# Performance work log

Measured on AMD Instinct MI355X. Metric: run time of the kernel, lower is better.

The kernel has to match this reference:

```python
import jax, jax.numpy as jnp
import numpy as np

C = 256

def _conv1x1(x, w, b):
    # x: [B,C,H,W], w: [O,I], b: [O]  (1x1 conv == pointwise GEMM over channels)
    return jnp.einsum('oi,bihw->bohw', w, x) + b[None, :, None, None]

def setup_inputs() -> dict:
    key = jax.random.key(0)
    ks = jax.random.split(key, 9)
    s = 1.0 / np.sqrt(C)
    x = jax.random.normal(ks[0], (16, C, 64, 64), dtype=jnp.float32)
    wf = jax.random.uniform(ks[1], (C, C), jnp.float32, -s, s)
    bf = jax.random.uniform(ks[2], (C,), jnp.float32, -s, s)
    wg = jax.random.uniform(ks[3], (C, C), jnp.float32, -s, s)
    bg = jax.random.uniform(ks[4], (C,), jnp.float32, -s, s)
    wh = jax.random.uniform(ks[5], (C, C), jnp.float32, -s, s)
    bh = jax.random.uniform(ks[6], (C,), jnp.float32, -s, s)
    wv = jax.random.uniform(ks[7], (C, C), jnp.float32, -s, s)
    bv = jax.random.uniform(ks[8], (C,), jnp.float32, -s, s)
    return {"x": x, "wf": wf, "bf": bf, "wg": wg, "bg": bg,
            "wh": wh, "bh": bh, "wv": wv, "bv": bv}

def reference(x, wf, bf, wg, bg, wh, bh, wv, bv):
    fx = _conv1x1(x, wf, bf)              # [B,C,H,W]
    gx = _conv1x1(x, wg, bg)              # [B,C,H,W]
    # scores: fx^T @ gx over spatial H -> [B,C,W,W]
    scores = jnp.einsum('bchw,bchv->bcwv', fx, gx)
    attn = jax.nn.softmax(scores, axis=-1)  # softmax over last W dim
    hx = _conv1x1(x, wh, bh)              # [B,C,H,W]
    out = jnp.einsum('bchw,bcwv->bchv', hx, attn)  # hx @ attn -> [B,C,H,W]
    return _conv1x1(out, wv, bv)
```

## Files before the change

### kernel.cpp

```cpp
#include <hip/hip_runtime.h>
#include <math.h>

#define CH  256
#define SPA 4096
#define BB  16
#define PLANE 16777216

typedef _Float16 f16x8 __attribute__((ext_vector_type(8)));
typedef _Float16 f16x4 __attribute__((ext_vector_type(4)));
typedef float    f32x4 __attribute__((ext_vector_type(4)));

__device__ __forceinline__ void gload16(const void* g, void* l) {
    __builtin_amdgcn_global_load_lds(
        (const __attribute__((address_space(1))) unsigned int*)g,
        (__attribute__((address_space(3))) unsigned int*)l, 16, 0, 0);
}

__global__ __launch_bounds__(256) void xpose_kernel(
    const float* __restrict__ src, _Float16* __restrict__ dst)
{
    __shared__ float T[64][65];
    const int t  = threadIdx.x;
    const int b  = blockIdx.x >> 8;
    const int st = (blockIdx.x >> 2) & 63;
    const int rt = blockIdx.x & 3;
    const int s0 = st << 6, r0 = rt << 6;

    #pragma unroll
    for (int p = 0; p < 4; ++p) {
        int k = (t >> 4) + (p << 4);
        float4 v = *(const float4*)(src + (((size_t)((b << 8) + r0 + k)) << 12)
                                        + s0 + ((t & 15) << 2));
        T[k][((t & 15) << 2) + 0] = v.x;
        T[k][((t & 15) << 2) + 1] = v.y;
        T[k][((t & 15) << 2) + 2] = v.z;
        T[k][((t & 15) << 2) + 3] = v.w;
    }
    __syncthreads();

    const int s  = t >> 2;
    const int kg = (t & 3) << 4;
    const size_t obase = (((size_t)((b << 12) + s0 + s)) << 8) + r0 + kg;

    f16x8 h0, h1;
    #pragma unroll
    for (int i = 0; i < 16; ++i) {
        _Float16 hv = (_Float16)T[kg + i][s];
        if (i < 8) h0[i] = hv; else h1[i - 8] = hv;
    }
    *(f16x8*)(dst + obase)     = h0;
    *(f16x8*)(dst + obase + 8) = h1;
}

__global__ __launch_bounds__(256) void cpose_kernel(
    const _Float16* __restrict__ src, _Float16* __restrict__ dst)
{
    __shared__ _Float16 T[64][68];
    const int t  = threadIdx.x;
    const int b  = blockIdx.x >> 8;
    const int st = (blockIdx.x >> 2) & 63;
    const int ct = blockIdx.x & 3;
    const int s0 = st << 6, c0 = ct << 6;

    #pragma unroll
    for (int p = 0; p < 4; ++p) {
        int fi = (p << 8) + t;
        int r = fi >> 4, s4 = (fi & 15) << 2;
        f16x4 v = *(const f16x4*)(src + (((size_t)((b << 8) + c0 + r)) << 12) + s0 + s4);
        *(f16x4*)&T[r][s4] = v;
    }
    __syncthreads();

    const int s  = t >> 2;
    const int cg = (t & 3) << 4;
    f16x8 h0, h1;
    #pragma unroll
    for (int i = 0; i < 16; ++i) {
        _Float16 hv = T[cg + i][s];
        if (i < 8) h0[i] = hv; else h1[i - 8] = hv;
    }
    const size_t obase = (((size_t)((b << 12) + s0 + s)) << 8) + c0 + cg;
    *(f16x8*)(dst + obase)     = h0;
    *(f16x8*)(dst + obase + 8) = h1;
}

__global__ __launch_bounds__(256) void wcvt_kernel(
    const float* __restrict__ w0, const float* __restrict__ w1,
    const float* __restrict__ w2, const float* __restrict__ w3,
    _Float16* __restrict__ dst)
{
    const int idx = blockIdx.x * 256 + threadIdx.x;
    dst[idx]             = (_Float16)w0[idx];
    dst[65536 + idx]     = (_Float16)w1[idx];
    dst[131072 + idx]    = (_Float16)w2[idx];
    dst[196608 + idx]    = (_Float16)w3[idx];
}

__global__ __launch_bounds__(256) void gemm_fgh_kernel(
    const _Float16* __restrict__ xT, const _Float16* __restrict__ wc,
    const float* __restrict__ bias0, const float* __restrict__ bias1,
    const float* __restrict__ bias2, _Float16* __restrict__ outp)
{
    __shared__ _Float16 S[10240];
    _Float16* sA = S;

    const int tid = threadIdx.x;
    const int w = tid >> 6, lane = tid & 63, q = lane >> 4, li = lane & 15;
    const int r_ = blockIdx.x;
    const int ot    = r_ & 3;
    const int stile = (r_ >> 2) & 31;
    const int b     = r_ >> 7;
    const int s0 = stile << 7, o0 = ot << 6;

    const float* biases[3] = {bias0, bias1, bias2};

    f32x4 acc[3][4][2];
    #pragma unroll
    for (int m = 0; m < 3; ++m)
        #pragma unroll
        for (int t2 = 0; t2 < 4; ++t2)
            #pragma unroll
            for (int u = 0; u < 2; ++u) acc[m][t2][u] = (f32x4){0.f, 0.f, 0.f, 0.f};

    const int rr = tid >> 2;
    const int cc = (tid & 3) << 3;

    const int n0 = (w & 1) << 5;
    const int m0 = (w >> 1) << 6;

    for (int kb = 0; kb < CH; kb += 32) {
        __syncthreads();
        {
            const size_t ga = (((size_t)((b << 12) + s0 + rr)) << 8) + kb + cc;
            gload16(xT + ga, sA + tid * 8);
            gload16(xT + ga + (64ull << 8), sA + 2048 + tid * 8);
            #pragma unroll
            for (int m = 0; m < 3; ++m) {
                const size_t gb = (((size_t)(o0 + rr)) << 8) + m * 65536 + kb + cc;
                gload16(wc + gb, S + 4096 + m * 2048 + tid * 8);
            }
        }
        __syncthreads();

        f16x8 a[4];
        #pragma unroll
        for (int t2 = 0; t2 < 4; ++t2)
            a[t2] = *(const f16x8*)(sA + (m0 + (t2 << 4) + li) * 32 + (q << 3));

        #pragma unroll
        for (int m = 0; m < 3; ++m) {
            const _Float16* sB = S + 4096 + m * 2048;
            f16x8 b0 = *(const f16x8*)(sB + (n0 + li) * 32 + (q << 3));
            f16x8 b1 = *(const f16x8*)(sB + (n0 + 16 + li) * 32 + (q << 3));
            #pragma unroll
            for (int t2 = 0; t2 < 4; ++t2) {
                acc[m][t2][0] = __builtin_amdgcn_mfma_f32_16x16x32_f16(a[t2], b0, acc[m][t2][0], 0, 0, 0);
                acc[m][t2][1] = __builtin_amdgcn_mfma_f32_16x16x32_f16(a[t2], b1, acc[m][t2][1], 0, 0, 0);
            }
        }
    }

    #pragma unroll
    for (int m = 0; m < 3; ++m) {
        _Float16* ob = outp + (size_t)m * PLANE;
        #pragma unroll
        for (int u = 0; u < 2; ++u) {
            const int o = o0 + n0 + (u << 4) + li;
            const float bz = biases[m][o];
            #pragma unroll
            for (int t2 = 0; t2 < 4; ++t2) {
                const int s = s0 + m0 + (t2 << 4) + (q << 2);
                const size_t off = (((size_t)((b << 8) + o)) << 12) + s;
                f32x4 v = acc[m][t2][u];
                f16x4 pv;
                pv[0] = (_Float16)(v[0] + bz); pv[1] = (_Float16)(v[1] + bz);
                pv[2] = (_Float16)(v[2] + bz); pv[3] = (_Float16)(v[3] + bz);
                *(f16x4*)(ob + off) = pv;
            }
        }
    }
}

__global__ __launch_bounds__(256) void gemm16_kernel(
    const _Float16* __restrict__ xT, const _Float16* __restrict__ wp,
    const float* __restrict__ bias, float* __restrict__ outp)
{
    __shared__ _Float16 S[8192];
    _Float16* sA = S;
    _Float16* sB = S + 4096;

    const int tid = threadIdx.x;
    const int w = tid >> 6, lane = tid & 63, quad = lane >> 4, li = lane & 15;
    const int wx = w & 1, wy = w >> 1;
    const int r_ = blockIdx.x;
    const int ot    = r_ & 1;
    const int stile = (r_ >> 1) & 31;
    const int b     = r_ >> 6;
    const int s0 = stile << 7, o0 = ot << 7;

    f32x4 acc[4][4];
    #pragma unroll
    for (int t2 = 0; t2 < 4; ++t2)
        #pragma unroll
        for (int u = 0; u < 4; ++u) acc[t2][u] = (f32x4){0.f, 0.f, 0.f, 0.f};

    const int rr = lane >> 2, cc = (lane & 3) << 3;

    for (int kb = 0; kb < CH; kb += 32) {
        __syncthreads();
        #pragma unroll
        for (int j = 0; j < 32; j += 16) {
            const int r = (w << 5) + j + rr;
            const size_t ga = (((size_t)((b << 12) + s0 + r)) << 8) + kb + cc;
            const size_t gb = ((size_t)(o0 + r) << 8) + kb + cc;
            const int lo_ = ((w << 5) + j) * 32 + lane * 8;
            gload16(xT + ga, sA + lo_);
            gload16(wp + gb, sB + lo_);
        }
        __syncthreads();

        f16x8 a[4], bfr[4];
        #pragma unroll
        for (int t2 = 0; t2 < 4; ++t2) {
            a[t2]   = *(const f16x8*)(sA + ((wy << 6) + (t2 << 4) + li) * 32 + (quad << 3));
            bfr[t2] = *(const f16x8*)(sB + ((wx << 6) + (t2 << 4) + li) * 32 + (quad << 3));
        }
        #pragma unroll
        for (int t2 = 0; t2 < 4; ++t2)
            #pragma unroll
            for (int u = 0; u < 4; ++u)
                acc[t2][u] = __builtin_amdgcn_mfma_f32_16x16x32_f16(a[t2], bfr[u], acc[t2][u], 0, 0, 0);
    }

    #pragma unroll
    for (int u = 0; u < 4; ++u) {
        const int o = o0 + (wx << 6) + (u << 4) + li;
        const float bz = bias[o];
        #pragma unroll
        for (int t2 = 0; t2 < 4; ++t2) {
            const int s = s0 + (wy << 6) + (t2 << 4) + (quad << 2);
            const size_t off = (((size_t)((b << 8) + o)) << 12) + s;
            f32x4 v = acc[t2][u];
            float4 pv = {v[0] + bz, v[1] + bz, v[2] + bz, v[3] + bz};
            *(float4*)(outp + off) = pv;
        }
    }
}

__global__ __launch_bounds__(256) void attn_mfma_kernel(
    const _Float16* __restrict__ fx, const _Float16* __restrict__ gx,
    const _Float16* __restrict__ hx, _Float16* __restrict__ ob)
{
    __shared__ _Float16 L[23040];
    const int FT = 0, GT = 4608, HM = 9216;
    const int FR = 13824, GR = 18432;
    const int PT = 13824;

    const int t = threadIdx.x;
    const int wave = t >> 6, lane = t & 63, q = lane >> 4, li = lane & 15;
    const int bc = blockIdx.x;
    const _Float16* Fp = fx + (size_t)bc * SPA;
    const _Float16* Gp = gx + (size_t)bc * SPA;
    const _Float16* Hp = hx + (size_t)bc * SPA;
    _Float16* Op = ob + (size_t)bc * SPA;

    #pragma unroll
    for (int p = 0; p < 2; ++p) {
        int ci = t + (p << 8);
        int h = ci >> 3, w8 = (ci & 7) << 3;
        *(f16x8*)&L[FR + h * 72 + w8] = *(const f16x8*)(Fp + h * 64 + w8);
        *(f16x8*)&L[GR + h * 72 + w8] = *(const f16x8*)(Gp + h * 64 + w8);
        *(f16x8*)&L[HM + h * 72 + w8] = *(const f16x8*)(Hp + h * 64 + w8);
    }
    __syncthreads();

    {
        const int src = (wave < 2) ? FR : GR;
        const int dst = (wave < 2) ? FT : GT;
        const int mtb = (wave & 1) << 1;
        f16x8 id0, id1;
        #pragma unroll
        for (int j = 0; j < 8; ++j) {
            id0[j] = (_Float16)(((q << 3) + j == li)      ? 1.0f : 0.0f);
            id1[j] = (_Float16)(((q << 3) + j == li + 16) ? 1.0f : 0.0f);
        }
        #pragma unroll
        for (int mi = 0; mi < 2; ++mi) {
            const int mt = mtb + mi;
            f16x8 a0 = *(const f16x8*)&L[src + (mt * 16 + li) * 72 + (q << 3)];
            f16x8 a1 = *(const f16x8*)&L[src + (mt * 16 + li) * 72 + 32 + (q << 3)];
            #pragma unroll
            for (int nt = 0; nt < 4; ++nt) {
                f32x4 d = {0.f, 0.f, 0.f, 0.f};
                d = __builtin_amdgcn_mfma_f32_16x16x32_f16(
                        (nt < 2) ? a0 : a1, (nt & 1) ? id1 : id0, d, 0, 0, 0);
                f16x4 e;
                e[0] = (_Float16)d[0]; e[1] = (_Float16)d[1];
                e[2] = (_Float16)d[2]; e[3] = (_Float16)d[3];
                *(f16x4*)&L[dst + (nt * 16 + li) * 72 + mt * 16 + (q << 2)] = e;
            }
        }
    }
    __syncthreads();

    {
        f16x8 a0 = *(const f16x8*)&L[FT + (wave * 16 + li) * 72 + (q << 3)];
        f16x8 a1 = *(const f16x8*)&L[FT + (wave * 16 + li) * 72 + 32 + (q << 3)];
        f32x4 s_[4];
        #pragma unroll
        for (int nt = 0; nt < 4; ++nt) {
            f16x8 b0 = *(const f16x8*)&L[GT + (nt * 16 + li) * 72 + (q << 3)];
            f16x8 b1 = *(const f16x8*)&L[GT + (nt * 16 + li) * 72 + 32 + (q << 3)];
            f32x4 acc = {0.f, 0.f, 0.f, 0.f};
            acc = __builtin_amdgcn_mfma_f32_16x16x32_f16(a0, b0, acc, 0, 0, 0);
            acc = __builtin_amdgcn_mfma_f32_16x16x32_f16(a1, b1, acc, 0, 0, 0);
            s_[nt] = acc;
        }
        float mx[4], sm[4];
        #pragma unroll
        for (int r = 0; r < 4; ++r) {
            float m0 = fmaxf(fmaxf(s_[0][r], s_[1][r]), fmaxf(s_[2][r], s_[3][r]));
            m0 = fmaxf(m0, __shfl_xor(m0, 1));
            m0 = fmaxf(m0, __shfl_xor(m0, 2));
            m0 = fmaxf(m0, __shfl_xor(m0, 4));
            m0 = fmaxf(m0, __shfl_xor(m0, 8));
            mx[r] = m0;
        }
        #pragma unroll
        for (int nt = 0; nt < 4; ++nt)
            #pragma unroll
            for (int r = 0; r < 4; ++r)
                s_[nt][r] = __expf(s_[nt][r] - mx[r]);
        #pragma unroll
        for (int r = 0; r < 4; ++r) {
            float s0 = (s_[0][r] + s_[1][r]) + (s_[2][r] + s_[3][r]);
            s0 += __shfl_xor(s0, 1);
            s0 += __shfl_xor(s0, 2);
            s0 += __shfl_xor(s0, 4);
            s0 += __shfl_xor(s0, 8);
            sm[r] = 1.f / s0;
        }
        #pragma unroll
        for (int nt = 0; nt < 4; ++nt) {
            const int v  = nt * 16 + li;
            const int sw = ((v >> 3) & 7) << 3;
            #pragma unroll
            for (int r = 0; r < 4; ++r) {
                const int w = wave * 16 + (q << 2) + r;
                L[PT + v * 72 + (w ^ sw)] = (_Float16)(s_[nt][r] * sm[r]);
            }
        }
    }
    __syncthreads();

    {
        f16x8 a0 = *(const f16x8*)&L[HM + (wave * 16 + li) * 72 + (q << 3)];
        f16x8 a1 = *(const f16x8*)&L[HM + (wave * 16 + li) * 72 + 32 + (q << 3)];
        #pragma unroll
        for (int nt = 0; nt < 4; ++nt) {
            const int v  = nt * 16 + li;
            const int sw = ((v >> 3) & 7) << 3;
            f16x8 b0 = *(const f16x8*)&L[PT + v * 72 + ((q << 3) ^ sw)];
            f16x8 b1 = *(const f16x8*)&L[PT + v * 72 + ((32 + (q << 3)) ^ sw)];
            f32x4 acc = {0.f, 0.f, 0.f, 0.f};
            acc = __builtin_amdgcn_mfma_f32_16x16x32_f16(a0, b0, acc, 0, 0, 0);
            acc = __builtin_amdgcn_mfma_f32_16x16x32_f16(a1, b1, acc, 0, 0, 0);
            #pragma unroll
            for (int r = 0; r < 4; ++r)
                Op[(wave * 16 + (q << 2) + r) * 64 + v] = (_Float16)acc[r];
        }
    }
}

extern "C" void kernel_launch(void* const* d_in, const int* in_sizes, int n_in,
                              void* d_out, int out_size, void* d_ws, size_t ws_size,
                              hipStream_t stream)
{
    const float* x  = (const float*)d_in[0];
    const float* wf = (const float*)d_in[1];
    const float* bf = (const float*)d_in[2];
    const float* wg = (const float*)d_in[3];
    const float* bg = (const float*)d_in[4];
    const float* wh = (const float*)d_in[5];
    const float* bh = (const float*)d_in[6];
    const float* wv = (const float*)d_in[7];
    const float* bv = (const float*)d_in[8];

    char* base = (char*)d_ws;
    const size_t MB = 1ull << 20;
    _Float16* xT  = (_Float16*)base;
    _Float16* fxb = (_Float16*)(base + 32 * MB);
    _Float16* ob  = (_Float16*)(base + 128 * MB);
    _Float16* obT = (_Float16*)base;
    _Float16* wc  = (_Float16*)(base + 160 * MB);

    _Float16* gxb = fxb + PLANE;
    _Float16* hxb = gxb + PLANE;

    dim3 blk(256);
    xpose_kernel<<<4096, blk, 0, stream>>>(x, xT);
    wcvt_kernel<<<256, blk, 0, stream>>>(wf, wg, wh, wv, wc);

    gemm_fgh_kernel<<<2048, blk, 0, stream>>>(xT, wc, bf, bg, bh, fxb);

    attn_mfma_kernel<<<4096, blk, 0, stream>>>(fxb, gxb, hxb, ob);

    cpose_kernel<<<4096, blk, 0, stream>>>(ob, obT);

    gemm16_kernel<<<1024, blk, 0, stream>>>(obT, wc + 196608, bv, (float*)d_out);
}
```

Measured before the change: 251.2 us.

## Double-buffer LDS in 1x1-conv GEMMs with XOR swizzle and block remap

Both pointwise-conv GEMM kernels now ping-pong two LDS buffers so the global-to-LDS loads for the next K slice overlap the MFMA work on the current one, with a single waitcnt plus barrier per step. LDS columns are XOR-swizzled on both store and read to reduce bank conflicts on the fragment loads. Block indices are remapped so consecutive blocks are spread across batches and tiles, which changes cache and XCD locality. The cost is double the LDS per block, which may lower occupancy.

```diff
diff --git a/kernel.cpp b/kernel.cpp
--- a/kernel.cpp
+++ b/kernel.cpp
@@ -101,12 +101,12 @@
     const float* __restrict__ bias0, const float* __restrict__ bias1,
     const float* __restrict__ bias2, _Float16* __restrict__ outp)
 {
-    __shared__ _Float16 S[10240];
-    _Float16* sA = S;
+    __shared__ _Float16 S[2][10240];
 
     const int tid = threadIdx.x;
     const int w = tid >> 6, lane = tid & 63, q = lane >> 4, li = lane & 15;
-    const int r_ = blockIdx.x;
+
+    const int r_ = ((blockIdx.x & 7) << 8) + (blockIdx.x >> 3);
     const int ot    = r_ & 3;
     const int stile = (r_ >> 2) & 31;
     const int b     = r_ >> 7;
@@ -123,42 +123,56 @@
             for (int u = 0; u < 2; ++u) acc[m][t2][u] = (f32x4){0.f, 0.f, 0.f, 0.f};
 
     const int rr = tid >> 2;
-    const int cc = (tid & 3) << 3;
+    const int cs = (((tid & 3) ^ ((rr >> 1) & 3)) << 3);
 
     const int n0 = (w & 1) << 5;
     const int m0 = (w >> 1) << 6;
-
-    for (int kb = 0; kb < CH; kb += 32) {
-        __syncthreads();
-        {
-            const size_t ga = (((size_t)((b << 12) + s0 + rr)) << 8) + kb + cc;
-            gload16(xT + ga, sA + tid * 8);
-            gload16(xT + ga + (64ull << 8), sA + 2048 + tid * 8);
-            #pragma unroll
-            for (int m = 0; m < 3; ++m) {
-                const size_t gb = (((size_t)(o0 + rr)) << 8) + m * 65536 + kb + cc;
-                gload16(wc + gb, S + 4096 + m * 2048 + tid * 8);
-            }
-        }
-        __syncthreads();
-
+    const int sw = (li >> 1) & 3;
+
+    auto STAGE = [&](_Float16* sA, int kb) {
+        const size_t ga = (((size_t)((b << 12) + s0 + rr)) << 8) + kb + cs;
+        gload16(xT + ga, sA + tid * 8);
+        gload16(xT + ga + (64ull << 8), sA + 2048 + tid * 8);
+        #pragma unroll
+        for (int m = 0; m < 3; ++m) {
+            const size_t gb = (((size_t)(o0 + rr)) << 8) + m * 65536 + kb + cs;
+            gload16(wc + gb, sA + 4096 + m * 2048 + tid * 8);
+        }
+    };
+
+    auto COMPUTE = [&](const _Float16* sA) {
         f16x8 a[4];
         #pragma unroll
         for (int t2 = 0; t2 < 4; ++t2)
-            a[t2] = *(const f16x8*)(sA + (m0 + (t2 << 4) + li) * 32 + (q << 3));
+            a[t2] = *(const f16x8*)(sA + (m0 + (t2 << 4) + li) * 32 + ((q ^ sw) << 3));
 
         #pragma unroll
         for (int m = 0; m < 3; ++m) {
-            const _Float16* sB = S + 4096 + m * 2048;
-            f16x8 b0 = *(const f16x8*)(sB + (n0 + li) * 32 + (q << 3));
-            f16x8 b1 = *(const f16x8*)(sB + (n0 + 16 + li) * 32 + (q << 3));
+            const _Float16* sB = sA + 4096 + m * 2048;
+            f16x8 b0 = *(const f16x8*)(sB + (n0 + li) * 32 + ((q ^ sw) << 3));
+            f16x8 b1 = *(const f16x8*)(sB + (n0 + 16 + li) * 32 + ((q ^ sw) << 3));
             #pragma unroll
             for (int t2 = 0; t2 < 4; ++t2) {
                 acc[m][t2][0] = __builtin_amdgcn_mfma_f32_16x16x32_f16(a[t2], b0, acc[m][t2][0], 0, 0, 0);
                 acc[m][t2][1] = __builtin_amdgcn_mfma_f32_16x16x32_f16(a[t2], b1, acc[m][t2][1], 0, 0, 0);
             }
         }
-    }
+    };
+
+    STAGE(S[0], 0);
+    asm volatile("s_waitcnt vmcnt(0)" ::: "memory");
+    __builtin_amdgcn_s_barrier();
+
+    int cur = 0;
+    #pragma unroll 1
+    for (int ks = 0; ks < 7; ++ks) {
+        STAGE(S[cur ^ 1], (ks + 1) << 5);
+        COMPUTE(S[cur]);
+        asm volatile("s_waitcnt vmcnt(0)" ::: "memory");
+        __builtin_amdgcn_s_barrier();
+        cur ^= 1;
+    }
+    COMPUTE(S[cur]);
 
     #pragma unroll
     for (int m = 0; m < 3; ++m) {
@@ -185,14 +199,13 @@
     const _Float16* __restrict__ xT, const _Float16* __restrict__ wp,
     const float* __restrict__ bias, float* __restrict__ outp)
 {
-    __shared__ _Float16 S[8192];
-    _Float16* sA = S;
-    _Float16* sB = S + 4096;
+    __shared__ _Float16 S[2][8192];
 
     const int tid = threadIdx.x;
     const int w = tid >> 6, lane = tid & 63, quad = lane >> 4, li = lane & 15;
     const int wx = w & 1, wy = w >> 1;
-    const int r_ = blockIdx.x;
+
+    const int r_ = ((blockIdx.x & 7) << 7) + (blockIdx.x >> 3);
     const int ot    = r_ & 1;
     const int stile = (r_ >> 1) & 31;
     const int b     = r_ >> 6;
@@ -204,33 +217,50 @@
         #pragma unroll
         for (int u = 0; u < 4; ++u) acc[t2][u] = (f32x4){0.f, 0.f, 0.f, 0.f};
 
-    const int rr = lane >> 2, cc = (lane & 3) << 3;
-
-    for (int kb = 0; kb < CH; kb += 32) {
-        __syncthreads();
+    const int rr = lane >> 2;
+    const int cs = (((lane & 3) ^ ((rr >> 1) & 3)) << 3);
+    const int sw = (li >> 1) & 3;
+
+    auto STAGE = [&](_Float16* sAB, int kb) {
         #pragma unroll
         for (int j = 0; j < 32; j += 16) {
             const int r = (w << 5) + j + rr;
-            const size_t ga = (((size_t)((b << 12) + s0 + r)) << 8) + kb + cc;
-            const size_t gb = ((size_t)(o0 + r) << 8) + kb + cc;
+            const size_t ga = (((size_t)((b << 12) + s0 + r)) << 8) + kb + cs;
+            const size_t gb = ((size_t)(o0 + r) << 8) + kb + cs;
             const int lo_ = ((w << 5) + j) * 32 + lane * 8;
-            gload16(xT + ga, sA + lo_);
-            gload16(wp + gb, sB + lo_);
-        }
-        __syncthreads();
-
+            gload16(xT + ga, sAB + lo_);
+            gload16(wp + gb, sAB + 4096 + lo_);
+        }
+    };
+
+    auto COMPUTE = [&](const _Float16* sAB) {
         f16x8 a[4], bfr[4];
         #pragma unroll
         for (int t2 = 0; t2 < 4; ++t2) {
-            a[t2]   = *(const f16x8*)(sA + ((wy << 6) + (t2 << 4) + li) * 32 + (quad << 3));
-            bfr[t2] = *(const f16x8*)(sB + ((wx << 6) + (t2 << 4) + li) * 32 + (quad << 3));
+            a[t2]   = *(const f16x8*)(sAB + ((wy << 6) + (t2 << 4) + li) * 32 + ((quad ^ sw) << 3));
+            bfr[t2] = *(const f16x8*)(sAB + 4096 + ((wx << 6) + (t2 << 4) + li) * 32 + ((quad ^ sw) << 3));
         }
         #pragma unroll
         for (int t2 = 0; t2 < 4; ++t2)
             #pragma unroll
             for (int u = 0; u < 4; ++u)
                 acc[t2][u] = __builtin_amdgcn_mfma_f32_16x16x32_f16(a[t2], bfr[u], acc[t2][u], 0, 0, 0);
-    }
+    };
+
+    STAGE(S[0], 0);
+    asm volatile("s_waitcnt vmcnt(0)" ::: "memory");
+    __builtin_amdgcn_s_barrier();
+
+    int cur = 0;
+    #pragma unroll 1
+    for (int ks = 0; ks < 7; ++ks) {
+        STAGE(S[cur ^ 1], (ks + 1) << 5);
+        COMPUTE(S[cur]);
+        asm volatile("s_waitcnt vmcnt(0)" ::: "memory");
+        __builtin_amdgcn_s_barrier();
+        cur ^= 1;
+    }
+    COMPUTE(S[cur]);
 
     #pragma unroll
     for (int u = 0; u < 4; ++u) {
```

Result: slower. 259.6 us (+3.4%).
